# Performance work log

Measured on AMD Instinct MI355X. Metric: run time of the kernel, lower is better.

The kernel has to match this reference:

```python
import jax, jax.numpy as jnp
import numpy as np
from jax import lax

B, C, H, W = 2, 96, 96, 96
N = 8            # d_state
R = C // 16      # dt_rank = 6
K = 4            # scan directions


def _gn(x, g, b, eps=1e-5):
    # GroupNorm(num_groups=1): normalize over (C,H,W) per sample, per-channel affine
    mu = jnp.mean(x, axis=(1, 2, 3), keepdims=True)
    var = jnp.var(x, axis=(1, 2, 3), keepdims=True)
    xn = (x - mu) * jax.lax.rsqrt(var + eps)
    return xn * g[None, :, None, None] + b[None, :, None, None]


def _conv1x1(x, w, b):
    return jnp.einsum('bchw,oc->bohw', x, w) + b[None, :, None, None]


def _ss2d(x, xproj_w, dt_w, dt_b, A_log, Ds):
    # x: [B,C,H,W]. 4-directional selective scan (VMamba SS2D core).
    Bn, Cc, Hh, Ww = x.shape
    L = Hh * Ww
    x_hw = x.reshape(Bn, Cc, L)                                   # row-major
    x_wh = jnp.transpose(x, (0, 1, 3, 2)).reshape(Bn, Cc, L)      # col-major
    xs = jnp.stack([x_hw, x_wh, x_hw[..., ::-1], x_wh[..., ::-1]], axis=1)  # [B,K,C,L]
    xdbl = jnp.einsum('bkcl,kdc->bkdl', xs, xproj_w)              # [B,K,R+2N,L]
    dts, Bs, Cs = jnp.split(xdbl, [R, R + N], axis=2)             # [B,K,R,L],[B,K,N,L],[B,K,N,L]
    dts = jax.nn.softplus(jnp.einsum('bkrl,kcr->bkcl', dts, dt_w) + dt_b[None, :, :, None])  # [B,K,C,L]
    A = -jnp.exp(A_log)                                           # [K,C,N]
    dA = jnp.exp(dts[:, :, :, None, :] * A[None, :, :, :, None])                    # [B,K,C,N,L]
    dBx = dts[:, :, :, None, :] * Bs[:, :, None, :, :] * xs[:, :, :, None, :]       # [B,K,C,N,L]

    def comb(e1, e2):
        a1, b1 = e1
        a2, b2 = e2
        return a1 * a2, a2 * b1 + b2

    _, hs = lax.associative_scan(comb, (dA, dBx), axis=-1)        # h_t = dA_t*h_{t-1} + dBx_t
    ys = jnp.einsum('bkcnl,bknl->bkcl', hs, Cs) + Ds[None, :, :, None] * xs
    y0 = ys[:, 0]
    y1 = jnp.transpose(ys[:, 1].reshape(Bn, Cc, Ww, Hh), (0, 1, 3, 2)).reshape(Bn, Cc, L)
    y2 = ys[:, 2][..., ::-1]
    y3 = jnp.transpose(ys[:, 3][..., ::-1].reshape(Bn, Cc, Ww, Hh), (0, 1, 3, 2)).reshape(Bn, Cc, L)
    return (y0 + y1 + y2 + y3).reshape(Bn, Cc, Hh, Ww)


def setup_inputs() -> dict:
    key = jax.random.key(0)
    ks = jax.random.split(key, 12)
    f = lambda k, sh: jax.random.normal(k, sh, jnp.float32) * 0.02
    return {
        'x': jax.random.normal(ks[0], (B, C, H, W), jnp.float32),
        'ln_g': jnp.ones((C,), jnp.float32), 'ln_b': jnp.zeros((C,), jnp.float32),
        'p1_w': f(ks[1], (C, C)), 'p1_b': jnp.zeros((C,), jnp.float32),
        'p2_w': f(ks[2], (C, C)), 'p2_b': jnp.zeros((C,), jnp.float32),
        'dw_w': f(ks[3], (C, 1, 3, 3)), 'dw_b': jnp.zeros((C,), jnp.float32),
        'xproj_w': f(ks[4], (K, R + 2 * N, C)),
        'dt_w': f(ks[5], (K, C, R)), 'dt_b': f(ks[6], (K, C)),
        'A_log': jnp.log(jnp.broadcast_to(jnp.arange(1, N + 1, dtype=jnp.float32), (K, C, N))),
        'Ds': jnp.ones((K, C), jnp.float32),
        'n2_g': jnp.ones((C,), jnp.float32), 'n2_b': jnp.zeros((C,), jnp.float32),
        'ca_w1': f(ks[7], (C // 8, C)), 'ca_b1': jnp.zeros((C // 8,), jnp.float32),
        'ca_w2': f(ks[8], (C, C // 8)), 'ca_b2': jnp.zeros((C,), jnp.float32),
    }


def reference(x, ln_g, ln_b, p1_w, p1_b, p2_w, p2_b, dw_w, dw_b,
              xproj_w, dt_w, dt_b, A_log, Ds, n2_g, n2_b,
              ca_w1, ca_b1, ca_w2, ca_b2):
    h = _gn(x, ln_g, ln_b)
    a = jax.nn.silu(_conv1x1(h, p1_w, p1_b))                       # path 1
    b = _conv1x1(h, p2_w, p2_b)                                    # path 2
    b = lax.conv_general_dilated(b, dw_w, (1, 1), ((1, 1), (1, 1)),
                                 feature_group_count=C,
                                 dimension_numbers=('NCHW', 'OIHW', 'NCHW'))
    b = b + dw_b[None, :, None, None]
    b = jax.nn.silu(b)
    b = _ss2d(b, xproj_w, dt_w, dt_b, A_log, Ds)
    b = _gn(b, n2_g, n2_b)
    y = a * b
    # channel attention (SE-style, reduction 8)
    s = jnp.mean(y, axis=(2, 3))                                   # [B,C]
    z = jax.nn.relu(s @ ca_w1.T + ca_b1)
    attn = jax.nn.sigmoid(z @ ca_w2.T + ca_b2)
    y = y * attn[:, :, None, None]
    return x + y
```

## Files before the change

### kernel.cpp

```cpp
#include <hip/hip_runtime.h>
#include <hip/hip_bf16.h>
#include <cmath>
#include <cstdint>

constexpr int B_ = 2, C_ = 96, H_ = 96, W_ = 96, L_ = H_ * W_;
constexpr int N_ = 8, R_ = 6, K_ = 4, D_ = R_ + 2 * N_;
constexpr int CH_ = 128, G_ = L_ / CH_;
constexpr int JS_ = 4, SEG_ = CH_ / JS_;
constexpr int S_ = G_ * JS_;
constexpr float EPS_ = 1e-5f;

__device__ __forceinline__ float silu_f(float v) { return v / (1.f + __expf(-v)); }
__device__ __forceinline__ float softplus_f(float t) {
    return fmaxf(t, 0.f) + __logf(1.f + __expf(-fabsf(t)));
}

__device__ __forceinline__ void block_reduce2(float& a, float& b) {
    #pragma unroll
    for (int o = 32; o; o >>= 1) { a += __shfl_xor(a, o); b += __shfl_xor(b, o); }
    __shared__ float la[4], lb[4];
    int wid = threadIdx.x >> 6;
    if ((threadIdx.x & 63) == 0) { la[wid] = a; lb[wid] = b; }
    __syncthreads();
    if (threadIdx.x == 0) { a = la[0] + la[1] + la[2] + la[3]; b = lb[0] + lb[1] + lb[2] + lb[3]; }
}

__device__ __forceinline__ void block_reduce4(float& a, float& b, float& c, float& d) {
    #pragma unroll
    for (int o = 32; o; o >>= 1) {
        a += __shfl_xor(a, o); b += __shfl_xor(b, o);
        c += __shfl_xor(c, o); d += __shfl_xor(d, o);
    }
    __shared__ float ls[4][4];
    int wid = threadIdx.x >> 6;
    if ((threadIdx.x & 63) == 0) { ls[wid][0] = a; ls[wid][1] = b; ls[wid][2] = c; ls[wid][3] = d; }
    __syncthreads();
    if (threadIdx.x == 0) {
        a = ls[0][0] + ls[1][0] + ls[2][0] + ls[3][0];
        b = ls[0][1] + ls[1][1] + ls[2][1] + ls[3][1];
        c = ls[0][2] + ls[1][2] + ls[2][2] + ls[3][2];
        d = ls[0][3] + ls[1][3] + ls[2][3] + ls[3][3];
    }
}

__global__ __launch_bounds__(256) void stats_kernel(const float* __restrict__ in,
                                                    float* __restrict__ stats) {
    int b = blockIdx.y;
    const float* p = in + (size_t)b * ((size_t)C_ * L_);
    float s = 0.f, s2 = 0.f;
    const int total = C_ * L_;
    for (int i = blockIdx.x * 256 + threadIdx.x; i < total; i += gridDim.x * 256) {
        float v = p[i];
        s += v;
        s2 = fmaf(v, v, s2);
    }
    block_reduce2(s, s2);
    if (threadIdx.x == 0) {
        atomicAdd(&stats[2 * b], s);
        atomicAdd(&stats[2 * b + 1], s2);
    }
}

__global__ __launch_bounds__(192) void prep_kernel(
    const float* __restrict__ lng, const float* __restrict__ lnb,
    const float* __restrict__ w1, const float* __restrict__ w2,
    float* __restrict__ wmt, float* __restrict__ pq) {
    int t = threadIdx.x;
    int mat = t / 96, o = t % 96;
    const float* w = (mat == 0 ? w1 : w2) + o * C_;
    float* dst = wmt + ((size_t)(mat * 12 + o / 8) * C_) * 8 + (o % 8);
    float P = 0.f, Q = 0.f;
    for (int c = 0; c < C_; ++c) {
        float wv = w[c];
        float g = lng[c];
        P = fmaf(lnb[c], wv, P);
        Q = fmaf(g, wv, Q);
        dst[c * 8] = g * wv;
    }
    pq[mat * 192 + o] = P;
    pq[mat * 192 + 96 + o] = Q;
}

__global__ __launch_bounds__(256) void conv1x1_kernel(
    const float* __restrict__ x, const float* __restrict__ stats,
    const float* __restrict__ wmt, const float* __restrict__ pq,
    const float* __restrict__ b1, const float* __restrict__ b2,
    float* __restrict__ a, float* __restrict__ bpre) {
    constexpr int OG = 8;
    int b = blockIdx.z, by = blockIdx.y;
    int o0 = by * OG;
    int l = blockIdx.x * 256 + threadIdx.x;

    constexpr float inv = 1.f / (float)(C_ * L_);
    float mu = stats[2 * b] * inv;
    float var = stats[2 * b + 1] * inv - mu * mu;
    float rs = rsqrtf(var + EPS_);

    __shared__ float s1[C_][OG], s2[C_][OG];
    const float* w1p = wmt + ((size_t)(0 * 12 + by) * C_) * 8;
    const float* w2p = wmt + ((size_t)(1 * 12 + by) * C_) * 8;
    for (int i = threadIdx.x; i < C_ * OG / 4; i += 256) {
        ((float4*)s1)[i] = ((const float4*)w1p)[i];
        ((float4*)s2)[i] = ((const float4*)w2p)[i];
    }
    __syncthreads();

    const float* xb = x + (size_t)b * C_ * L_ + l;
    float acc1[OG], acc2[OG];
    #pragma unroll
    for (int j = 0; j < OG; ++j) { acc1[j] = 0.f; acc2[j] = 0.f; }
    for (int c = 0; c < C_; ++c) {
        float xv = xb[(size_t)c * L_];
        float4 wa = *(const float4*)&s1[c][0];
        float4 wb = *(const float4*)&s1[c][4];
        float4 wc = *(const float4*)&s2[c][0];
        float4 wd = *(const float4*)&s2[c][4];
        acc1[0] = fmaf(xv, wa.x, acc1[0]); acc1[1] = fmaf(xv, wa.y, acc1[1]);
        acc1[2] = fmaf(xv, wa.z, acc1[2]); acc1[3] = fmaf(xv, wa.w, acc1[3]);
        acc1[4] = fmaf(xv, wb.x, acc1[4]); acc1[5] = fmaf(xv, wb.y, acc1[5]);
        acc1[6] = fmaf(xv, wb.z, acc1[6]); acc1[7] = fmaf(xv, wb.w, acc1[7]);
        acc2[0] = fmaf(xv, wc.x, acc2[0]); acc2[1] = fmaf(xv, wc.y, acc2[1]);
        acc2[2] = fmaf(xv, wc.z, acc2[2]); acc2[3] = fmaf(xv, wc.w, acc2[3]);
        acc2[4] = fmaf(xv, wd.x, acc2[4]); acc2[5] = fmaf(xv, wd.y, acc2[5]);
        acc2[6] = fmaf(xv, wd.z, acc2[6]); acc2[7] = fmaf(xv, wd.w, acc2[7]);
    }
    float murs = mu * rs;
    #pragma unroll
    for (int j = 0; j < OG; ++j) {
        int o = o0 + j;
        size_t oo = ((size_t)(b * C_ + o)) * L_ + l;
        float be1 = b1[o] + pq[o] - murs * pq[96 + o];
        float be2 = b2[o] + pq[192 + o] - murs * pq[288 + o];
        a[oo] = silu_f(fmaf(rs, acc1[j], be1));
        bpre[oo] = fmaf(rs, acc2[j], be2);
    }
}

__global__ __launch_bounds__(256) void dwt_kernel(const float* __restrict__ bp,
                                                  const float* __restrict__ wgt,
                                                  const float* __restrict__ bias,
                                                  float* __restrict__ u,
                                                  float* __restrict__ u_t) {
    int stripe = blockIdx.x, c = blockIdx.y, b = blockIdx.z;
    int h0 = stripe * 48;
    __shared__ float in_s[50][96];
    __shared__ float out_s[48][97];
    const float* in = bp + ((size_t)(b * C_ + c)) * L_;
    for (int idx = threadIdx.x; idx < 50 * 96; idx += 256) {
        int r = idx / 96, w = idx % 96;
        int hh = h0 - 1 + r;
        in_s[r][w] = (hh >= 0 && hh < 96) ? in[hh * 96 + w] : 0.f;
    }
    __syncthreads();
    const float* kw = wgt + c * 9;
    float k0 = kw[0], k1 = kw[1], k2 = kw[2], k3 = kw[3], k4 = kw[4],
          k5 = kw[5], k6 = kw[6], k7 = kw[7], k8 = kw[8];
    float bs = bias[c];
    float* up = u + ((size_t)(b * C_ + c)) * L_;
    for (int idx = threadIdx.x; idx < 48 * 96; idx += 256) {
        int r = idx / 96, w = idx % 96;
        int ri = r + 1;
        bool wl = (w > 0), wr = (w < 95);
        float acc = bs;
        acc = fmaf(wl ? in_s[ri - 1][w - 1] : 0.f, k0, acc);
        acc = fmaf(in_s[ri - 1][w], k1, acc);
        acc = fmaf(wr ? in_s[ri - 1][w + 1] : 0.f, k2, acc);
        acc = fmaf(wl ? in_s[ri][w - 1] : 0.f, k3, acc);
        acc = fmaf(in_s[ri][w], k4, acc);
        acc = fmaf(wr ? in_s[ri][w + 1] : 0.f, k5, acc);
        acc = fmaf(wl ? in_s[ri + 1][w - 1] : 0.f, k6, acc);
        acc = fmaf(in_s[ri + 1][w], k7, acc);
        acc = fmaf(wr ? in_s[ri + 1][w + 1] : 0.f, k8, acc);
        float v = silu_f(acc);
        up[(h0 + r) * 96 + w] = v;
        out_s[r][w] = v;
    }
    __syncthreads();
    float* tp = u_t + ((size_t)(b * C_ + c)) * L_;
    for (int idx = threadIdx.x; idx < 96 * 48; idx += 256) {
        int w = idx / 48, r = idx % 48;
        tp[w * 96 + h0 + r] = out_s[r][w];
    }
}

__global__ __launch_bounds__(256) void proj_kernel(
    const float* __restrict__ u, const float* __restrict__ u_t,
    const float* __restrict__ xproj,
    float* __restrict__ dts, float* __restrict__ Bsb, float* __restrict__ Csb) {
    int b = blockIdx.z, k = blockIdx.y;
    int pos = threadIdx.x & 63, cg = threadIdx.x >> 6;
    int l = blockIdx.x * 64 + pos;

    __shared__ float sxp[C_][24];
    __shared__ float red[D_][4][64];
    for (int i = threadIdx.x; i < D_ * C_; i += 256) {
        int d = i / C_, c = i % C_;
        sxp[c][d] = xproj[(k * D_ + d) * C_ + c];
    }
    __syncthreads();

    const float* src = ((k & 1) ? u_t : u) + (size_t)b * C_ * L_;
    int posIdx = (k < 2) ? l : (L_ - 1 - l);
    const float* sp = src + (size_t)(cg * 24) * L_ + posIdx;

    float acc[D_];
    #pragma unroll
    for (int d = 0; d < D_; ++d) acc[d] = 0.f;
    #pragma unroll 4
    for (int ci = 0; ci < 24; ++ci) {
        int c = cg * 24 + ci;
        float xv = sp[(size_t)ci * L_];
        float w[22];
        *(float4*)&w[0]  = *(const float4*)&sxp[c][0];
        *(float4*)&w[4]  = *(const float4*)&sxp[c][4];
        *(float4*)&w[8]  = *(const float4*)&sxp[c][8];
        *(float4*)&w[12] = *(const float4*)&sxp[c][12];
        *(float4*)&w[16] = *(const float4*)&sxp[c][16];
        *(float2*)&w[20] = *(const float2*)&sxp[c][20];
        #pragma unroll
        for (int d = 0; d < D_; ++d) acc[d] = fmaf(xv, w[d], acc[d]);
    }
    #pragma unroll
    for (int d = 0; d < D_; ++d) red[d][cg][pos] = acc[d];
    __syncthreads();

    if (cg == 0) {
        #pragma unroll
        for (int r = 0; r < R_; ++r) {
            float s = red[r][0][pos] + red[r][1][pos] + red[r][2][pos] + red[r][3][pos];
            dts[((size_t)((b * K_ + k) * R_ + r)) * L_ + l] = s;
        }
    } else if (cg == 1) {
        #pragma unroll
        for (int n = 0; n < N_; ++n) {
            int d = R_ + n;
            float s = red[d][0][pos] + red[d][1][pos] + red[d][2][pos] + red[d][3][pos];
            Bsb[((size_t)((b * K_ + k) * N_ + n)) * L_ + l] = s;
        }
    } else if (cg == 2) {
        #pragma unroll
        for (int n = 0; n < N_; ++n) {
            int d = R_ + N_ + n;
            float s = red[d][0][pos] + red[d][1][pos] + red[d][2][pos] + red[d][3][pos];
            Csb[((size_t)((b * K_ + k) * N_ + n)) * L_ + l] = s;
        }
    }
}


__global__ __launch_bounds__(192) void scan1_kernel(
    const float* __restrict__ dts, const float* __restrict__ dtw,
    const float* __restrict__ dtbv, const float* __restrict__ Bs,
    const float* __restrict__ u, const float* __restrict__ u_t,
    const float* __restrict__ A_log,
    float* __restrict__ carA, float* __restrict__ carB) {
    int g = blockIdx.x >> 1, chalf = blockIdx.x & 1;
    int k = blockIdx.y, b = blockIdx.z;
    int c0 = chalf * 48;
    const int t = threadIdx.x;
    const int l0 = g * CH_;

    __shared__ float u_s[48][132];
    __shared__ float B_s[128][12];
    __shared__ float T_s[128][8];

    const float* usrc = ((k & 1) ? u_t : u) + (size_t)b * C_ * L_ + (size_t)c0 * L_;
    if (k < 2) {
        for (int idx = t; idx < 48 * 32; idx += 192) {
            int c2 = idx >> 5, q = idx & 31;
            *(float4*)&u_s[c2][q * 4] = *(const float4*)(usrc + (size_t)c2 * L_ + l0 + q * 4);
        }
    } else {
        for (int idx = t; idx < 48 * 32; idx += 192) {
            int c2 = idx >> 5, q = idx & 31;
            float4 v = *(const float4*)(usrc + (size_t)c2 * L_ + (L_ - l0 - q * 4 - 4));
            u_s[c2][q * 4 + 0] = v.w; u_s[c2][q * 4 + 1] = v.z;
            u_s[c2][q * 4 + 2] = v.y; u_s[c2][q * 4 + 3] = v.x;
        }
    }
    const float* Bg = Bs + ((size_t)(b * K_ + k)) * N_ * L_ + l0;
    for (int idx = t; idx < 8 * 32; idx += 192) {
        int n = idx >> 5, q = idx & 31;
        float4 v = *(const float4*)(Bg + (size_t)n * L_ + q * 4);
        B_s[q * 4 + 0][n] = v.x; B_s[q * 4 + 1][n] = v.y;
        B_s[q * 4 + 2][n] = v.z; B_s[q * 4 + 3][n] = v.w;
    }
    const float* Tg = dts + ((size_t)(b * K_ + k)) * R_ * L_ + l0;
    for (int idx = t; idx < 6 * 32; idx += 192) {
        int r = idx >> 5, q = idx & 31;
        float4 v = *(const float4*)(Tg + (size_t)r * L_ + q * 4);
        T_s[q * 4 + 0][r] = v.x; T_s[q * 4 + 1][r] = v.y;
        T_s[q * 4 + 2][r] = v.z; T_s[q * 4 + 3][r] = v.w;
    }
    __syncthreads();

    int cc = t % 48, j = t / 48;
    int c = c0 + cc;
    float A[N_];
    #pragma unroll
    for (int n = 0; n < N_; ++n) A[n] = -__expf(A_log[(k * C_ + c) * N_ + n]);
    float wdt[R_];
    #pragma unroll
    for (int r = 0; r < R_; ++r) wdt[r] = dtw[(k * C_ + c) * R_ + r];
    float bdt = dtbv[k * C_ + c];

    float ap[N_], h[N_];
    #pragma unroll
    for (int n = 0; n < N_; ++n) { ap[n] = 1.f; h[n] = 0.f; }
    int i0 = j * SEG_;
    for (int ii = 0; ii < SEG_; ii += 4) {
        float4 x4 = *(float4*)&u_s[cc][i0 + ii];
        float xx[4] = {x4.x, x4.y, x4.z, x4.w};
        #pragma unroll
        for (int s = 0; s < 4; ++s) {
            int i = i0 + ii + s;
            float4 t4 = *(float4*)&T_s[i][0];
            float2 t2 = *(float2*)&T_s[i][4];
            float tt = bdt;
            tt = fmaf(t4.x, wdt[0], tt); tt = fmaf(t4.y, wdt[1], tt);
            tt = fmaf(t4.z, wdt[2], tt); tt = fmaf(t4.w, wdt[3], tt);
            tt = fmaf(t2.x, wdt[4], tt); tt = fmaf(t2.y, wdt[5], tt);
            float d = softplus_f(tt);
            float dx = d * xx[s];
            float4 ba = *(float4*)&B_s[i][0];
            float4 bb = *(float4*)&B_s[i][4];
            float bv[8] = {ba.x, ba.y, ba.z, ba.w, bb.x, bb.y, bb.z, bb.w};
            #pragma unroll
            for (int n = 0; n < N_; ++n) {
                float da = __expf(d * A[n]);
                ap[n] *= da;
                h[n] = fmaf(da, h[n], bv[n] * dx);
            }
        }
    }
    size_t sidx = (((size_t)((b * K_ + k) * C_ + c)) * S_ + (g * JS_ + j)) * N_;
    #pragma unroll
    for (int n = 0; n < N_; ++n) { carA[sidx + n] = ap[n]; carB[sidx + n] = h[n]; }
}

__global__ __launch_bounds__(256) void scan2_kernel(const float* __restrict__ carA,
                                                    const float* __restrict__ carB,
                                                    float* __restrict__ hinit) {
    int tid = blockIdx.x * 256 + threadIdx.x;
    if (tid >= B_ * K_ * C_ * N_) return;
    int n = tid & 7;
    size_t rowb = (size_t)(tid >> 3) * S_;
    float h = 0.f;
    for (int s = 0; s < S_; s += 8) {
        float av[8], bv[8];
        #pragma unroll
        for (int q = 0; q < 8; ++q) {
            size_t idx = (rowb + s + q) * N_ + n;
            av[q] = carA[idx]; bv[q] = carB[idx];
        }
        #pragma unroll
        for (int q = 0; q < 8; ++q) {
            size_t idx = (rowb + s + q) * N_ + n;
            hinit[idx] = h;
            h = fmaf(av[q], h, bv[q]);
        }
    }
}

__global__ __launch_bounds__(192) void scan3_kernel(
    const float* __restrict__ dts, const float* __restrict__ dtw,
    const float* __restrict__ dtbv, const float* __restrict__ Bs,
    const float* __restrict__ Cs, const float* __restrict__ u,
    const float* __restrict__ u_t, const float* __restrict__ A_log,
    const float* __restrict__ Dsv, const float* __restrict__ hinit,
    float* __restrict__ ydir) {
    int g = blockIdx.x >> 1, chalf = blockIdx.x & 1;
    int k = blockIdx.y, b = blockIdx.z;
    int c0 = chalf * 48;
    const int t = threadIdx.x;
    const int l0 = g * CH_;

    __shared__ float u_s[48][132];
    __shared__ float B_s[128][12];
    __shared__ float C_s[128][12];
    __shared__ float T_s[128][8];

    const float* usrc = ((k & 1) ? u_t : u) + (size_t)b * C_ * L_ + (size_t)c0 * L_;
    if (k < 2) {
        for (int idx = t; idx < 48 * 32; idx += 192) {
            int c2 = idx >> 5, q = idx & 31;
            *(float4*)&u_s[c2][q * 4] = *(const float4*)(usrc + (size_t)c2 * L_ + l0 + q * 4);
        }
    } else {
        for (int idx = t; idx < 48 * 32; idx += 192) {
            int c2 = idx >> 5, q = idx & 31;
            float4 v = *(const float4*)(usrc + (size_t)c2 * L_ + (L_ - l0 - q * 4 - 4));
            u_s[c2][q * 4 + 0] = v.w; u_s[c2][q * 4 + 1] = v.z;
            u_s[c2][q * 4 + 2] = v.y; u_s[c2][q * 4 + 3] = v.x;
        }
    }
    const float* Bg = Bs + ((size_t)(b * K_ + k)) * N_ * L_ + l0;
    const float* Cg = Cs + ((size_t)(b * K_ + k)) * N_ * L_ + l0;
    for (int idx = t; idx < 8 * 32; idx += 192) {
        int n = idx >> 5, q = idx & 31;
        float4 v = *(const float4*)(Bg + (size_t)n * L_ + q * 4);
        B_s[q * 4 + 0][n] = v.x; B_s[q * 4 + 1][n] = v.y;
        B_s[q * 4 + 2][n] = v.z; B_s[q * 4 + 3][n] = v.w;
        float4 w = *(const float4*)(Cg + (size_t)n * L_ + q * 4);
        C_s[q * 4 + 0][n] = w.x; C_s[q * 4 + 1][n] = w.y;
        C_s[q * 4 + 2][n] = w.z; C_s[q * 4 + 3][n] = w.w;
    }
    const float* Tg = dts + ((size_t)(b * K_ + k)) * R_ * L_ + l0;
    for (int idx = t; idx < 6 * 32; idx += 192) {
        int r = idx >> 5, q = idx & 31;
        float4 v = *(const float4*)(Tg + (size_t)r * L_ + q * 4);
        T_s[q * 4 + 0][r] = v.x; T_s[q * 4 + 1][r] = v.y;
        T_s[q * 4 + 2][r] = v.z; T_s[q * 4 + 3][r] = v.w;
    }
    __syncthreads();

    int cc = t % 48, j = t / 48;
    int c = c0 + cc;
    float A[N_];
    #pragma unroll
    for (int n = 0; n < N_; ++n) A[n] = -__expf(A_log[(k * C_ + c) * N_ + n]);
    float wdt[R_];
    #pragma unroll
    for (int r = 0; r < R_; ++r) wdt[r] = dtw[(k * C_ + c) * R_ + r];
    float bdt = dtbv[k * C_ + c];
    float Dv = Dsv[k * C_ + c];

    float h[N_];
    size_t sidx = (((size_t)((b * K_ + k) * C_ + c)) * S_ + (g * JS_ + j)) * N_;
    #pragma unroll
    for (int n = 0; n < N_; ++n) h[n] = hinit[sidx + n];

    int i0 = j * SEG_;
    for (int ii = 0; ii < SEG_; ii += 4) {
        float4 x4 = *(float4*)&u_s[cc][i0 + ii];
        float xx[4] = {x4.x, x4.y, x4.z, x4.w};
        #pragma unroll
        for (int s = 0; s < 4; ++s) {
            int i = i0 + ii + s;
            float4 t4 = *(float4*)&T_s[i][0];
            float2 t2 = *(float2*)&T_s[i][4];
            float tt = bdt;
            tt = fmaf(t4.x, wdt[0], tt); tt = fmaf(t4.y, wdt[1], tt);
            tt = fmaf(t4.z, wdt[2], tt); tt = fmaf(t4.w, wdt[3], tt);
            tt = fmaf(t2.x, wdt[4], tt); tt = fmaf(t2.y, wdt[5], tt);
            float d = softplus_f(tt);
            float dx = d * xx[s];
            float4 ba = *(float4*)&B_s[i][0];
            float4 bb = *(float4*)&B_s[i][4];
            float4 ca = *(float4*)&C_s[i][0];
            float4 cb = *(float4*)&C_s[i][4];
            float bv[8] = {ba.x, ba.y, ba.z, ba.w, bb.x, bb.y, bb.z, bb.w};
            float cv[8] = {ca.x, ca.y, ca.z, ca.w, cb.x, cb.y, cb.z, cb.w};
            float y = Dv * xx[s];
            #pragma unroll
            for (int n = 0; n < N_; ++n) {
                float da = __expf(d * A[n]);
                h[n] = fmaf(da, h[n], bv[n] * dx);
                y = fmaf(cv[n], h[n], y);
            }
            u_s[cc][i] = y;
        }
    }
    __syncthreads();
    float* yg = ydir + ((size_t)((b * K_ + k) * C_ + c0)) * L_ + l0;
    for (int idx = t; idx < 48 * 32; idx += 192) {
        int c2 = idx >> 5, q = idx & 31;
        *(float4*)(yg + (size_t)c2 * L_ + q * 4) = *(float4*)&u_s[c2][q * 4];
    }
}

__global__ __launch_bounds__(256) void merge_kernel(const float* __restrict__ ydir,
                                                    const float* __restrict__ a,
                                                    float* __restrict__ ysum,
                                                    float* __restrict__ stats) {
    int h0 = blockIdx.x * 32;
    int c = blockIdx.y, b = blockIdx.z;
    __shared__ float t1[96][33], t3[96][33];
    const float* y0p = ydir + ((size_t)((b * K_ + 0) * C_ + c)) * L_;
    const float* y1p = ydir + ((size_t)((b * K_ + 1) * C_ + c)) * L_;
    const float* y2p = ydir + ((size_t)((b * K_ + 2) * C_ + c)) * L_;
    const float* y3p = ydir + ((size_t)((b * K_ + 3) * C_ + c)) * L_;
    for (int idx = threadIdx.x; idx < 96 * 32; idx += 256) {
        int w = idx >> 5, hh = idx & 31;
        t1[w][hh] = y1p[w * 96 + h0 + hh];
        t3[w][hh] = y3p[L_ - 1 - (w * 96 + h0 + hh)];
    }
    __syncthreads();
    float s = 0.f, s2 = 0.f, m0 = 0.f, m1 = 0.f;
    float* yout = ysum + ((size_t)(b * C_ + c)) * L_;
    const float* ap = a + ((size_t)(b * C_ + c)) * L_;
    for (int idx = threadIdx.x; idx < 32 * 96; idx += 256) {
        int hh = idx / 96, w = idx % 96;
        int pix = (h0 + hh) * 96 + w;
        float v = y0p[pix] + y2p[L_ - 1 - pix] + t1[w][hh] + t3[w][hh];
        float av = ap[pix];
        yout[pix] = v;
        s += v;
        s2 = fmaf(v, v, s2);
        m0 += av;
        m1 = fmaf(av, v, m1);
    }
    block_reduce4(s, s2, m0, m1);
    if (threadIdx.x == 0) {
        atomicAdd(&stats[4 + 2 * b], s);
        atomicAdd(&stats[5 + 2 * b], s2);
        atomicAdd(&stats[16 + b * C_ + c], m0);
        atomicAdd(&stats[256 + b * C_ + c], m1);
    }
}

__global__ __launch_bounds__(128) void attn_kernel(
    const float* __restrict__ stats, const float* __restrict__ g2,
    const float* __restrict__ b2, const float* __restrict__ w1,
    const float* __restrict__ b1, const float* __restrict__ w2,
    const float* __restrict__ b2a, float* __restrict__ attn) {
    int b = blockIdx.x;
    constexpr float inv = 1.f / (float)(C_ * L_);
    float mu = stats[4 + 2 * b] * inv;
    float var = stats[5 + 2 * b] * inv - mu * mu;
    float rs = rsqrtf(var + EPS_);
    __shared__ float ss[C_];
    __shared__ float zz[12];
    int t = threadIdx.x;
    if (t < C_) {
        float M0 = stats[16 + b * C_ + t];
        float M1 = stats[256 + b * C_ + t];
        ss[t] = (g2[t] * rs * (M1 - mu * M0) + b2[t] * M0) * (1.f / (float)L_);
    }
    __syncthreads();
    if (t < 12) {
        float acc = b1[t];
        for (int c = 0; c < C_; ++c) acc = fmaf(w1[t * C_ + c], ss[c], acc);
        zz[t] = fmaxf(acc, 0.f);
    }
    __syncthreads();
    if (t < C_) {
        float acc = b2a[t];
        #pragma unroll
        for (int j = 0; j < 12; ++j) acc = fmaf(w2[t * 12 + j], zz[j], acc);
        attn[b * C_ + t] = 1.f / (1.f + __expf(-acc));
    }
}

__global__ __launch_bounds__(256) void final_kernel(const float* __restrict__ x,
                                                    const float* __restrict__ ysum,
                                                    const float* __restrict__ a,
                                                    const float* __restrict__ stats,
                                                    const float* __restrict__ g2,
                                                    const float* __restrict__ b2,
                                                    const float* __restrict__ attn,
                                                    float* __restrict__ out) {
    int b = blockIdx.z, c = blockIdx.y;
    int pix = blockIdx.x * 256 + threadIdx.x;
    constexpr float inv = 1.f / (float)(C_ * L_);
    float mu = stats[4 + 2 * b] * inv;
    float var = stats[5 + 2 * b] * inv - mu * mu;
    float rs = rsqrtf(var + EPS_);
    float gc = g2[c] * rs, bc = b2[c] - mu * rs * g2[c];
    float at = attn[b * C_ + c];
    size_t o = ((size_t)(b * C_ + c)) * L_ + pix;
    float bn = fmaf(ysum[o], gc, bc);
    out[o] = fmaf(a[o] * bn, at, x[o]);
}

extern "C" void kernel_launch(void* const* d_in, const int* in_sizes, int n_in,
                              void* d_out, int out_size, void* d_ws, size_t ws_size,
                              hipStream_t stream) {
    const float* x    = (const float*)d_in[0];
    const float* ln_g = (const float*)d_in[1];
    const float* ln_b = (const float*)d_in[2];
    const float* p1w  = (const float*)d_in[3];
    const float* p1b  = (const float*)d_in[4];
    const float* p2w  = (const float*)d_in[5];
    const float* p2b  = (const float*)d_in[6];
    const float* dww  = (const float*)d_in[7];
    const float* dwb  = (const float*)d_in[8];
    const float* xprj = (const float*)d_in[9];
    const float* dtw  = (const float*)d_in[10];
    const float* dtb  = (const float*)d_in[11];
    const float* Alog = (const float*)d_in[12];
    const float* Dsp  = (const float*)d_in[13];
    const float* n2g  = (const float*)d_in[14];
    const float* n2b  = (const float*)d_in[15];
    const float* caw1 = (const float*)d_in[16];
    const float* cab1 = (const float*)d_in[17];
    const float* caw2 = (const float*)d_in[18];
    const float* cab2 = (const float*)d_in[19];
    float* out = (float*)d_out;

    const size_t BCL = (size_t)B_ * C_ * L_ * sizeof(float);
    char* ws = (char*)d_ws;
    size_t off = 0;
    float* stats = (float*)(ws + off); off += 4096;
    float* wmt   = (float*)(ws + off); off += 2 * 12 * 96 * 8 * sizeof(float);
    float* pq    = (float*)(ws + off); off += 2 * 2 * 96 * sizeof(float);
    float* a     = (float*)(ws + off); off += BCL;
    float* bpre  = (float*)(ws + off); off += BCL;
    float* u     = (float*)(ws + off); off += BCL;
    float* u_t   = (float*)(ws + off); off += BCL;
    float* dts   = (float*)(ws + off); off += (size_t)B_ * K_ * R_ * L_ * sizeof(float);
    float* Bsb   = (float*)(ws + off); off += (size_t)B_ * K_ * N_ * L_ * sizeof(float);
    float* Csb   = (float*)(ws + off); off += (size_t)B_ * K_ * N_ * L_ * sizeof(float);
    float* carB  = (float*)(ws + off); off += (size_t)B_ * K_ * C_ * S_ * N_ * sizeof(float);
    float* hinit = (float*)(ws + off); off += (size_t)B_ * K_ * C_ * S_ * N_ * sizeof(float);
    float* ydir  = (float*)(ws + off); off += (size_t)B_ * K_ * C_ * L_ * sizeof(float);
    float* carA = bpre;
    float* ysum = u;
    float* attnv = stats + 512;

    hipMemsetAsync(stats, 0, 4096, stream);

    prep_kernel<<<1, 192, 0, stream>>>(ln_g, ln_b, p1w, p2w, wmt, pq);
    stats_kernel<<<dim3(432, 2), 256, 0, stream>>>(x, stats);
    conv1x1_kernel<<<dim3(36, 12, 2), 256, 0, stream>>>(x, stats, wmt, pq, p1b, p2b, a, bpre);
    dwt_kernel<<<dim3(2, 96, 2), 256, 0, stream>>>(bpre, dww, dwb, u, u_t);
    proj_kernel<<<dim3(144, 4, 2), 256, 0, stream>>>(u, u_t, xprj, dts, Bsb, Csb);
    scan1_kernel<<<dim3(2 * G_, K_, B_), 192, 0, stream>>>(dts, dtw, dtb, Bsb, u, u_t,
                                                           Alog, carA, carB);
    scan2_kernel<<<24, 256, 0, stream>>>(carA, carB, hinit);
    scan3_kernel<<<dim3(2 * G_, K_, B_), 192, 0, stream>>>(dts, dtw, dtb, Bsb, Csb, u, u_t,
                                                           Alog, Dsp, hinit, ydir);
    merge_kernel<<<dim3(3, 96, 2), 256, 0, stream>>>(ydir, a, ysum, stats);
    attn_kernel<<<2, 128, 0, stream>>>(stats, n2g, n2b, caw1, cab1, caw2, cab2, attnv);
    final_kernel<<<dim3(36, 96, 2), 256, 0, stream>>>(x, ysum, a, stats, n2g, n2b, attnv, out);
}
```

Before: 289.5 us.

## Fold weight prep into stats kernel, read conv weights directly, repad scan smem

Merges the single-block weight-prep kernel into the GroupNorm stats kernel as an extra block, which removes one kernel launch. The 1x1 conv kernel now reads its pre-transposed weights straight from global memory (uniform across the block) instead of staging them in shared memory with a barrier, and its channel loop is unrolled by 4. The scan kernels pad the u_s shared tile row to 133 floats to change the bank-conflict pattern. Risks are higher global or cache traffic for the weight reads and different LDS access behaviour.

```diff
diff --git a/kernel.cpp b/kernel.cpp
--- a/kernel.cpp
+++ b/kernel.cpp
@@ -43,13 +43,35 @@
     }
 }
 
-__global__ __launch_bounds__(256) void stats_kernel(const float* __restrict__ in,
-                                                    float* __restrict__ stats) {
+__global__ __launch_bounds__(256) void stats_prep_kernel(
+    const float* __restrict__ in, float* __restrict__ stats,
+    const float* __restrict__ lng, const float* __restrict__ lnb,
+    const float* __restrict__ w1, const float* __restrict__ w2,
+    float* __restrict__ wmt, float* __restrict__ pq) {
+    if (blockIdx.x == 432) {
+        if (blockIdx.y != 0) return;
+        int t = threadIdx.x;
+        if (t >= 192) return;
+        int mat = t / 96, o = t % 96;
+        const float* w = (mat == 0 ? w1 : w2) + o * C_;
+        float* dst = wmt + ((size_t)(mat * 12 + o / 8) * C_) * 8 + (o % 8);
+        float P = 0.f, Q = 0.f;
+        for (int c = 0; c < C_; ++c) {
+            float wv = w[c];
+            float g = lng[c];
+            P = fmaf(lnb[c], wv, P);
+            Q = fmaf(g, wv, Q);
+            dst[c * 8] = g * wv;
+        }
+        pq[mat * 192 + o] = P;
+        pq[mat * 192 + 96 + o] = Q;
+        return;
+    }
     int b = blockIdx.y;
     const float* p = in + (size_t)b * ((size_t)C_ * L_);
     float s = 0.f, s2 = 0.f;
     const int total = C_ * L_;
-    for (int i = blockIdx.x * 256 + threadIdx.x; i < total; i += gridDim.x * 256) {
+    for (int i = blockIdx.x * 256 + threadIdx.x; i < total; i += 432 * 256) {
         float v = p[i];
         s += v;
         s2 = fmaf(v, v, s2);
@@ -59,26 +81,6 @@
         atomicAdd(&stats[2 * b], s);
         atomicAdd(&stats[2 * b + 1], s2);
     }
-}
-
-__global__ __launch_bounds__(192) void prep_kernel(
-    const float* __restrict__ lng, const float* __restrict__ lnb,
-    const float* __restrict__ w1, const float* __restrict__ w2,
-    float* __restrict__ wmt, float* __restrict__ pq) {
-    int t = threadIdx.x;
-    int mat = t / 96, o = t % 96;
-    const float* w = (mat == 0 ? w1 : w2) + o * C_;
-    float* dst = wmt + ((size_t)(mat * 12 + o / 8) * C_) * 8 + (o % 8);
-    float P = 0.f, Q = 0.f;
-    for (int c = 0; c < C_; ++c) {
-        float wv = w[c];
-        float g = lng[c];
-        P = fmaf(lnb[c], wv, P);
-        Q = fmaf(g, wv, Q);
-        dst[c * 8] = g * wv;
-    }
-    pq[mat * 192 + o] = P;
-    pq[mat * 192 + 96 + o] = Q;
 }
 
 __global__ __launch_bounds__(256) void conv1x1_kernel(
@@ -96,25 +98,20 @@
     float var = stats[2 * b + 1] * inv - mu * mu;
     float rs = rsqrtf(var + EPS_);
 
-    __shared__ float s1[C_][OG], s2[C_][OG];
-    const float* w1p = wmt + ((size_t)(0 * 12 + by) * C_) * 8;
-    const float* w2p = wmt + ((size_t)(1 * 12 + by) * C_) * 8;
-    for (int i = threadIdx.x; i < C_ * OG / 4; i += 256) {
-        ((float4*)s1)[i] = ((const float4*)w1p)[i];
-        ((float4*)s2)[i] = ((const float4*)w2p)[i];
-    }
-    __syncthreads();
+    const float4* w1q = (const float4*)(wmt + ((size_t)(0 * 12 + by) * C_) * 8);
+    const float4* w2q = (const float4*)(wmt + ((size_t)(1 * 12 + by) * C_) * 8);
 
     const float* xb = x + (size_t)b * C_ * L_ + l;
     float acc1[OG], acc2[OG];
     #pragma unroll
     for (int j = 0; j < OG; ++j) { acc1[j] = 0.f; acc2[j] = 0.f; }
+    #pragma unroll 4
     for (int c = 0; c < C_; ++c) {
         float xv = xb[(size_t)c * L_];
-        float4 wa = *(const float4*)&s1[c][0];
-        float4 wb = *(const float4*)&s1[c][4];
-        float4 wc = *(const float4*)&s2[c][0];
-        float4 wd = *(const float4*)&s2[c][4];
+        float4 wa = w1q[2 * c];
+        float4 wb = w1q[2 * c + 1];
+        float4 wc = w2q[2 * c];
+        float4 wd = w2q[2 * c + 1];
         acc1[0] = fmaf(xv, wa.x, acc1[0]); acc1[1] = fmaf(xv, wa.y, acc1[1]);
         acc1[2] = fmaf(xv, wa.z, acc1[2]); acc1[3] = fmaf(xv, wa.w, acc1[3]);
         acc1[4] = fmaf(xv, wb.x, acc1[4]); acc1[5] = fmaf(xv, wb.y, acc1[5]);
@@ -260,7 +257,7 @@
     const int t = threadIdx.x;
     const int l0 = g * CH_;
 
-    __shared__ float u_s[48][132];
+    __shared__ float u_s[48][133];
     __shared__ float B_s[128][12];
     __shared__ float T_s[128][8];
 
@@ -375,7 +372,7 @@
     const int t = threadIdx.x;
     const int l0 = g * CH_;
 
-    __shared__ float u_s[48][132];
+    __shared__ float u_s[48][133];
     __shared__ float B_s[128][12];
     __shared__ float C_s[128][12];
     __shared__ float T_s[128][8];
@@ -610,8 +607,8 @@
 
     hipMemsetAsync(stats, 0, 4096, stream);
 
-    prep_kernel<<<1, 192, 0, stream>>>(ln_g, ln_b, p1w, p2w, wmt, pq);
-    stats_kernel<<<dim3(432, 2), 256, 0, stream>>>(x, stats);
+    stats_prep_kernel<<<dim3(433, 2), 256, 0, stream>>>(x, stats, ln_g, ln_b,
+                                                        p1w, p2w, wmt, pq);
     conv1x1_kernel<<<dim3(36, 12, 2), 256, 0, stream>>>(x, stats, wmt, pq, p1b, p2b, a, bpre);
     dwt_kernel<<<dim3(2, 96, 2), 256, 0, stream>>>(bpre, dww, dwb, u, u_t);
     proj_kernel<<<dim3(144, 4, 2), 256, 0, stream>>>(u, u_t, xprj, dts, Bsb, Csb);
```

Result: faster. 281.1 us (-2.9%).
